# Kernel optimization log

Hardware: AMD Instinct MI355X
Metric: run time of the kernel (lower is better)

The kernel has to match this reference:

```python
import jax, jax.numpy as jnp
import numpy as np

M = 3  # vMF dimension (3D direction vectors)
KAPPA_SWITCH = 100.0


def _log_cmk_exact(kappa):
    """Exact log C_m(kappa) for m=3 via closed-form I_{1/2}(x)=sqrt(2/(pi x))*sinh(x).

    Matches LogCMK.forward: (m/2-1)*log(k) - log(iv(m/2-1,k)) - (m/2)*log(2*pi).
    Uses a numerically stable log-sinh: log(sinh k) = k + log1p(-exp(-2k)) - log 2.
    """
    log_sinh = kappa + jnp.log1p(-jnp.exp(-2.0 * kappa)) - jnp.log(2.0)
    log_iv = 0.5 * (jnp.log(2.0) - jnp.log(jnp.pi) - jnp.log(kappa)) + log_sinh
    return 0.5 * jnp.log(kappa) - log_iv - 1.5 * jnp.log(2.0 * jnp.pi)


def _log_cmk_approx(m, kappa):
    # [1812.04616] Sec 8.2 (with extra minus sign), as in the torch code.
    v = m / 2.0 - 0.5
    a = jnp.sqrt((v + 1.0) ** 2 + kappa ** 2)
    b = v - 1.0
    return -a + b * jnp.log(b + a)


def _log_cmk(m, kappa):
    ks = jnp.asarray(KAPPA_SWITCH, kappa.dtype)
    # continuity offset at the switch point
    offset = _log_cmk_approx(m, ks) - _log_cmk_exact(ks)
    return jnp.where(kappa < ks, _log_cmk_exact(kappa), _log_cmk_approx(m, kappa) - offset)


def setup_inputs() -> dict:
    key = jax.random.key(0)
    k1, k2 = jax.random.split(key)
    N, D = 8_000_000, M
    prediction = jax.random.normal(k1, (N, D), dtype=jnp.float32)
    t = jax.random.normal(k2, (N, D), dtype=jnp.float32)
    target = t / jnp.linalg.norm(t, axis=1, keepdims=True)  # unit direction targets
    return {"prediction": prediction, "target": target}


def reference(prediction, target):
    m = target.shape[1]
    kappa = jnp.linalg.norm(prediction, axis=1)            # [N]
    dotprod = jnp.sum(prediction * target, axis=1)          # [N]
    elements = -_log_cmk(m, kappa) - dotprod                # [N]
    return jnp.mean(elements)  # LossFunction.forward default (no weights, averaged)
```

## Files before the change

kernel.cpp:

```cpp
#include <hip/hip_runtime.h>
#include <math.h>

#define NTHR 256
#define MAXBLK 8192

__device__ __forceinline__ float vmf_elem(float x, float y, float z,
                                          float tx, float ty, float tz) {
    float k2  = fmaf(x, x, fmaf(y, y, z * z));
    float dot = fmaf(x, tx, fmaf(y, ty, z * tz));
    float k   = __builtin_amdgcn_sqrtf(k2);
    float e2k = __expf(-2.0f * k);
    float u   = fmaxf(1.0f - e2k, 1e-37f);
    float lr  = __logf(u * __builtin_amdgcn_rcpf(fmaxf(k, 1e-30f)));
    float nlc_small = k + lr + 1.8378770664093453f;
    float nlc_big   = __builtin_amdgcn_sqrtf(4.0f + k2) - 2.78729112f;
    float nlc = (k < 100.0f) ? nlc_small : nlc_big;
    return nlc - dot;
}

__global__ __launch_bounds__(NTHR) void vmf_partial_kernel(
    const float* __restrict__ pred, const float* __restrict__ targ,
    float* __restrict__ partial, int nchunk, int nrem, int nbase) {
    const float4* p4 = reinterpret_cast<const float4*>(pred);
    const float4* t4 = reinterpret_cast<const float4*>(targ);
    int tid    = blockIdx.x * blockDim.x + threadIdx.x;
    int stride = gridDim.x * blockDim.x;

    float acc = 0.0f;
    for (int c = tid; c < nchunk; c += stride) {
        int b = 6 * c;
        float4 p0 = p4[b + 0], p1 = p4[b + 1], p2 = p4[b + 2];
        float4 p3 = p4[b + 3], p5 = p4[b + 4], p6 = p4[b + 5];
        float4 t0 = t4[b + 0], t1 = t4[b + 1], t2 = t4[b + 2];
        float4 t3 = t4[b + 3], t5 = t4[b + 4], t6 = t4[b + 5];
        acc += vmf_elem(p0.x, p0.y, p0.z, t0.x, t0.y, t0.z);
        acc += vmf_elem(p0.w, p1.x, p1.y, t0.w, t1.x, t1.y);
        acc += vmf_elem(p1.z, p1.w, p2.x, t1.z, t1.w, t2.x);
        acc += vmf_elem(p2.y, p2.z, p2.w, t2.y, t2.z, t2.w);
        acc += vmf_elem(p3.x, p3.y, p3.z, t3.x, t3.y, t3.z);
        acc += vmf_elem(p3.w, p5.x, p5.y, t3.w, t5.x, t5.y);
        acc += vmf_elem(p5.z, p5.w, p6.x, t5.z, t5.w, t6.x);
        acc += vmf_elem(p6.y, p6.z, p6.w, t6.y, t6.z, t6.w);
    }
    if (tid == 0) {
        for (int r = 0; r < nrem; ++r) {
            int i = nbase + r;
            acc += vmf_elem(pred[3 * i], pred[3 * i + 1], pred[3 * i + 2],
                            targ[3 * i], targ[3 * i + 1], targ[3 * i + 2]);
        }
    }

    for (int off = 32; off > 0; off >>= 1)
        acc += __shfl_down(acc, off, 64);
    __shared__ float sdata[NTHR / 64];
    int lane = threadIdx.x & 63, wid = threadIdx.x >> 6;
    if (lane == 0) sdata[wid] = acc;
    __syncthreads();
    if (threadIdx.x == 0) {
        float s = 0.0f;
        #pragma unroll
        for (int w = 0; w < NTHR / 64; ++w) s += sdata[w];
        partial[blockIdx.x] = s;
    }
}

__global__ __launch_bounds__(NTHR) void vmf_final_kernel(
    const float* __restrict__ partial, float* __restrict__ out,
    int nblk, float invN) {
    float s = 0.0f;
    for (int i = threadIdx.x; i < nblk; i += NTHR) s += partial[i];
    for (int off = 32; off > 0; off >>= 1)
        s += __shfl_down(s, off, 64);
    __shared__ float sdata[NTHR / 64];
    int lane = threadIdx.x & 63, wid = threadIdx.x >> 6;
    if (lane == 0) sdata[wid] = s;
    __syncthreads();
    if (threadIdx.x == 0) {
        float tot = 0.0f;
        #pragma unroll
        for (int w = 0; w < NTHR / 64; ++w) tot += sdata[w];
        out[0] = tot * invN;
    }
}

extern "C" void kernel_launch(void* const* d_in, const int* in_sizes, int n_in,
                              void* d_out, int out_size, void* d_ws, size_t ws_size,
                              hipStream_t stream) {
    const float* pred = (const float*)d_in[0];
    const float* targ = (const float*)d_in[1];
    float* out = (float*)d_out;
    float* partial = (float*)d_ws;

    long long nrows = (long long)in_sizes[0] / 3;
    int nchunk = (int)(nrows / 8);
    int nrem   = (int)(nrows % 8);
    int nbase  = nchunk * 8;

    int blocks = (nchunk + NTHR - 1) / NTHR;
    if (blocks > MAXBLK) blocks = MAXBLK;
    if (blocks < 1) blocks = 1;

    vmf_partial_kernel<<<blocks, NTHR, 0, stream>>>(pred, targ, partial,
                                                    nchunk, nrem, nbase);
    vmf_final_kernel<<<1, NTHR, 0, stream>>>(partial, out, blocks,
                                             1.0f / (float)nrows);
}
```

Measured before the change: 208.4 us.

## Stage row tiles through LDS for fully coalesced float4 loads

```diff
diff --git a/kernel.cpp b/kernel.cpp
--- a/kernel.cpp
+++ b/kernel.cpp
@@ -2,7 +2,9 @@
 #include <math.h>
 
 #define NTHR 256
-#define MAXBLK 8192
+#define MAXBLK 1536
+#define TILE_ROWS 1024
+#define TILE_F4   768
 
 __device__ __forceinline__ float vmf_elem(float x, float y, float z,
                                           float tx, float ty, float tz) {
@@ -18,33 +20,40 @@
     return nlc - dot;
 }
 
+__device__ __forceinline__ float vmf_row(const float* r, const float* t) {
+    return vmf_elem(r[0], r[1], r[2], t[0], t[1], t[2]);
+}
+
 __global__ __launch_bounds__(NTHR) void vmf_partial_kernel(
     const float* __restrict__ pred, const float* __restrict__ targ,
-    float* __restrict__ partial, int nchunk, int nrem, int nbase) {
+    float* __restrict__ partial, int ntiles, int nrem, long long nbase) {
+    __shared__ float4 lp[TILE_F4];
+    __shared__ float4 lt[TILE_F4];
     const float4* p4 = reinterpret_cast<const float4*>(pred);
     const float4* t4 = reinterpret_cast<const float4*>(targ);
-    int tid    = blockIdx.x * blockDim.x + threadIdx.x;
-    int stride = gridDim.x * blockDim.x;
+    const int tid = threadIdx.x;
 
     float acc = 0.0f;
-    for (int c = tid; c < nchunk; c += stride) {
-        int b = 6 * c;
-        float4 p0 = p4[b + 0], p1 = p4[b + 1], p2 = p4[b + 2];
-        float4 p3 = p4[b + 3], p5 = p4[b + 4], p6 = p4[b + 5];
-        float4 t0 = t4[b + 0], t1 = t4[b + 1], t2 = t4[b + 2];
-        float4 t3 = t4[b + 3], t5 = t4[b + 4], t6 = t4[b + 5];
-        acc += vmf_elem(p0.x, p0.y, p0.z, t0.x, t0.y, t0.z);
-        acc += vmf_elem(p0.w, p1.x, p1.y, t0.w, t1.x, t1.y);
-        acc += vmf_elem(p1.z, p1.w, p2.x, t1.z, t1.w, t2.x);
-        acc += vmf_elem(p2.y, p2.z, p2.w, t2.y, t2.z, t2.w);
-        acc += vmf_elem(p3.x, p3.y, p3.z, t3.x, t3.y, t3.z);
-        acc += vmf_elem(p3.w, p5.x, p5.y, t3.w, t5.x, t5.y);
-        acc += vmf_elem(p5.z, p5.w, p6.x, t5.z, t5.w, t6.x);
-        acc += vmf_elem(p6.y, p6.z, p6.w, t6.y, t6.z, t6.w);
+    for (int tile = blockIdx.x; tile < ntiles; tile += gridDim.x) {
+        long long base = (long long)tile * TILE_F4;
+        __syncthreads();
+        lp[tid          ] = p4[base + tid          ];
+        lp[tid + NTHR   ] = p4[base + tid + NTHR   ];
+        lp[tid + 2*NTHR ] = p4[base + tid + 2*NTHR ];
+        lt[tid          ] = t4[base + tid          ];
+        lt[tid + NTHR   ] = t4[base + tid + NTHR   ];
+        lt[tid + 2*NTHR ] = t4[base + tid + 2*NTHR ];
+        __syncthreads();
+        float4 a0 = lp[3 * tid], a1 = lp[3 * tid + 1], a2 = lp[3 * tid + 2];
+        float4 b0 = lt[3 * tid], b1 = lt[3 * tid + 1], b2 = lt[3 * tid + 2];
+        acc += vmf_elem(a0.x, a0.y, a0.z, b0.x, b0.y, b0.z);
+        acc += vmf_elem(a0.w, a1.x, a1.y, b0.w, b1.x, b1.y);
+        acc += vmf_elem(a1.z, a1.w, a2.x, b1.z, b1.w, b2.x);
+        acc += vmf_elem(a2.y, a2.z, a2.w, b2.y, b2.z, b2.w);
     }
-    if (tid == 0) {
-        for (int r = 0; r < nrem; ++r) {
-            int i = nbase + r;
+    if (blockIdx.x == 0) {
+        for (int r = tid; r < nrem; r += NTHR) {
+            long long i = nbase + r;
             acc += vmf_elem(pred[3 * i], pred[3 * i + 1], pred[3 * i + 2],
                             targ[3 * i], targ[3 * i + 1], targ[3 * i + 2]);
         }
@@ -92,16 +101,14 @@
     float* partial = (float*)d_ws;
 
     long long nrows = (long long)in_sizes[0] / 3;
-    int nchunk = (int)(nrows / 8);
-    int nrem   = (int)(nrows % 8);
-    int nbase  = nchunk * 8;
+    int ntiles = (int)(nrows / TILE_ROWS);
+    int nrem   = (int)(nrows % TILE_ROWS);
+    long long nbase = (long long)ntiles * TILE_ROWS;
 
-    int blocks = (nchunk + NTHR - 1) / NTHR;
-    if (blocks > MAXBLK) blocks = MAXBLK;
-    if (blocks < 1) blocks = 1;
+    int blocks = ntiles < MAXBLK ? (ntiles > 0 ? ntiles : 1) : MAXBLK;
 
     vmf_partial_kernel<<<blocks, NTHR, 0, stream>>>(pred, targ, partial,
-                                                    nchunk, nrem, nbase);
+                                                    ntiles, nrem, nbase);
     vmf_final_kernel<<<1, NTHR, 0, stream>>>(partial, out, blocks,
-                                             1.0f / (float)nrows);
+                                             1.0f / (double)nrows);
 }
```

New measurement: 205.6 us. Within noise of the previous version (-1.4%).
